# Optimization experiments

Measured on AMD Instinct MI355X. Metric: run time of the kernel, lower is better.

The kernel has to match this reference:

```python
import jax, jax.numpy as jnp
import numpy as np

ITERS = 3

def squash(x, axis=-1):
    norm = jnp.linalg.norm(x, axis=axis, keepdims=True)
    scale = norm ** 2 / (1 + norm ** 2) / (norm + 1e-08)
    return scale * x

def setup_inputs() -> dict:
    key = jax.random.key(0)
    kx, kw = jax.random.split(key)
    x = jax.random.normal(kx, (64, 8000, 8), dtype=jnp.float32)
    W = 0.01 * jax.random.normal(kw, (10, 8000, 16, 8), dtype=jnp.float32)
    return {"x": x, "W": W}

def reference(x, W):
    # u_hat[b,o,i,d] = W[o,i,d,e] @ x[b,i,e]
    u_hat = jnp.einsum('oide,bie->boid', W, x)  # [B, O, I, D]
    temp_u_hat = jax.lax.stop_gradient(u_hat)
    B, O, I, D = u_hat.shape
    b = jnp.zeros((B, O, I, 1), dtype=u_hat.dtype)
    v = jnp.ones((B, O, D), dtype=u_hat.dtype)
    for i in range(ITERS):
        c = jax.nn.softmax(b, axis=1)  # over out_caps
        if i < ITERS - 1:
            s = (c * temp_u_hat).sum(axis=2)       # [B, O, D]
            v = squash(s)
            # agreement: u_hat . v over dim D
            b = b + jnp.einsum('boid,bod->boi', temp_u_hat, v)[..., None]
        else:
            s = (c * u_hat).sum(axis=2)
            v = squash(s)
    return v
```

## Files before the change

### kernel.cpp

```cpp
#include <hip/hip_runtime.h>
#include <hip/hip_fp16.h>
#include <math.h>

#define IN 8000
#define OC 10
#define NUNIT 1000
#define VACC_F (64 * OC * 16)
#define PART_H (64 * OC * 16)

#define REC_B   28672
#define REC_H   14336
#define XOFF_B  20480
#define XOFF_H  10240
#define REC_TOTAL_B ((size_t)NUNIT * REC_B)

#define SM_BYTES 41984

typedef __fp16 h2 __attribute__((ext_vector_type(2)));
typedef _Float16 half8 __attribute__((ext_vector_type(8)));
typedef float f32x16 __attribute__((ext_vector_type(16)));

__device__ __forceinline__ h2 asb(unsigned int v) { return __builtin_bit_cast(h2, v); }

__device__ __forceinline__ float dot2(h2 a, h2 b, float c) {
#if __has_builtin(__builtin_amdgcn_fdot2)
    return __builtin_amdgcn_fdot2(a, b, c, false);
#else
    return fmaf((float)a[0], (float)b[0], fmaf((float)a[1], (float)b[1], c));
#endif
}

__device__ __forceinline__ unsigned int pk_rn(float a, float b) {
    return __builtin_bit_cast(unsigned int, __float22half2_rn(make_float2(a, b)));
}

#define GLDS16(gp, lp) __builtin_amdgcn_global_load_lds(                      \
    (const __attribute__((address_space(1))) void*)(gp),                      \
    (__attribute__((address_space(3))) void*)(lp), 16, 0, 0)

__global__ __launch_bounds__(256) void caps_prep(
    const float* __restrict__ W, const float* __restrict__ x,
    __fp16* __restrict__ rec)
{
    const int t   = threadIdx.x;
    const int blk = blockIdx.x;
    if (blk < 1250) {
        const int gt = blk * 256 + t;
#pragma unroll
        for (int k = 0; k < 4; ++k) {
            int g  = gt + k * 320000;
            int u  = g / 1280;
            int r  = g - u * 1280;
            int il = r / 160;
            int rr = r - il * 160;
            int o  = rr >> 4;
            int d  = rr & 15;
            const float* ip = W + ((size_t)o * IN + (size_t)(u * 8 + il)) * 128 + d * 8;
            float4 f0 = *(const float4*)(ip);
            float4 f1 = *(const float4*)(ip + 4);
            uint4 pk = make_uint4(pk_rn(f0.x, f0.y), pk_rn(f0.z, f0.w),
                                  pk_rn(f1.x, f1.y), pk_rn(f1.z, f1.w));
            *(uint4*)(rec + (size_t)u * REC_H + il * 1280 + o * 128 + d * 8) = pk;
        }
    } else {
        const int u    = (blk - 1250) * 4 + (t >> 6);
        const int lane = t & 63;
#pragma unroll
        for (int il = 0; il < 8; ++il) {
            const float* ip = x + ((size_t)lane * IN + (size_t)(u * 8 + il)) * 8;
            float4 f0 = *(const float4*)(ip);
            float4 f1 = *(const float4*)(ip + 4);
            uint4 pk = make_uint4(pk_rn(f0.x, f0.y), pk_rn(f0.z, f0.w),
                                  pk_rn(f1.x, f1.y), pk_rn(f1.z, f1.w));
            *(uint4*)(rec + (size_t)u * REC_H + XOFF_H + il * 512 + lane * 8) = pk;
        }
    }
}

template<int UNIFORM>
__global__ __launch_bounds__(256, 3) void caps_pass(
    const __fp16* __restrict__ rec, const float* __restrict__ Vacc,
    __fp16* __restrict__ part)
{
    __shared__ __align__(16) unsigned char sm[SM_BYTES];
    __shared__ __align__(16) unsigned char zs[16];

    const int t    = threadIdx.x;
    const int w    = t >> 6;
    const int lane = t & 63;
    const int lo   = lane & 31;
    const int hi   = lane >> 5;
    const int bt   = w & 1;
    const int ph   = w >> 1;
    const int b    = bt * 32 + lo;

    if (t < 4) ((unsigned int*)zs)[t] = 0u;

    h2 vh[10][4];
    if (!UNIFORM) {
        const float* vp = Vacc + (size_t)b * (OC * 16);
        const float L2E = 1.44269504f;
#pragma unroll
        for (int o = 0; o < OC; ++o) {
            float4 fa = *(const float4*)(vp + o * 16 + 4 * hi);
            float4 fb = *(const float4*)(vp + o * 16 + 8 + 4 * hi);
            vh[o][0] = asb(pk_rn(fa.x * L2E, fa.y * L2E));
            vh[o][1] = asb(pk_rn(fa.z * L2E, fa.w * L2E));
            vh[o][2] = asb(pk_rn(fb.x * L2E, fb.y * L2E));
            vh[o][3] = asb(pk_rn(fb.z * L2E, fb.w * L2E));
        }
    }

    f32x16 acc[5];
    h2 acch[5][8];
    if (UNIFORM) {
#pragma unroll
        for (int op = 0; op < 5; ++op)
#pragma unroll
            for (int k = 0; k < 16; ++k) acc[op][k] = 0.f;
    } else {
#pragma unroll
        for (int op = 0; op < 5; ++op)
#pragma unroll
            for (int q = 0; q < 8; ++q) acch[op][q] = h2{(__fp16)0.f, (__fp16)0.f};
    }

    f32x16 zc;
#pragma unroll
    for (int k = 0; k < 16; ++k) zc[k] = 0.f;

    const int bid  = blockIdx.x;
    const int grid = gridDim.x;

    auto issue = [&](int st) {
        const char* g = (const char*)rec + (size_t)st * REC_B + (size_t)lane * 16;
#pragma unroll
        for (int c = 0; c < 7; ++c) {
            const int q = c * 4 + w;
            GLDS16(g + q * 1024, sm + q * 1024);
        }
    };

    bool first = true;
    for (int st = bid; st < NUNIT; st += grid) {
        if (!first) __syncthreads();
        issue(st);
        __syncthreads();
        first = false;

        const unsigned char* buf = sm;

        if (UNIFORM) {
#pragma unroll
            for (int ip = 0; ip < 2; ++ip) {
                const int il0 = ph * 4 + ip * 2;
                half8 xb = *(const half8*)(buf + XOFF_B + (il0 + hi) * 1024 + b * 16);
#pragma unroll
                for (int op = 0; op < 5; ++op) {
                    half8 av = *(const half8*)(buf + (il0 + hi) * 2560 + op * 512 + lo * 16);
                    acc[op] = __builtin_amdgcn_mfma_f32_32x32x16_f16(av, xb, acc[op], 0, 0, 0);
                }
            }
        } else {
#pragma unroll 1
            for (int u = 0; u < 4; ++u) {
                const int il = ph * 4 + u;
                const unsigned char* xaddr = (lane < 32)
                    ? (buf + XOFF_B + il * 1024 + b * 16)
                    : (const unsigned char*)zs;
                half8 xb = *(const half8*)xaddr;

                h2 uh2[5][8];
                float lgf[10];
#pragma unroll
                for (int op = 0; op < 5; ++op) {
                    half8 av = *(const half8*)(buf + il * 2560 + op * 512 + lo * 16);
                    f32x16 C = __builtin_amdgcn_mfma_f32_32x32x16_f16(av, xb, zc, 0, 0, 0);
#pragma unroll
                    for (int q = 0; q < 8; ++q)
                        uh2[op][q] = __builtin_amdgcn_cvt_pkrtz(C[2 * q], C[2 * q + 1]);
                    float l0 = 0.f, l1 = 0.f;
#pragma unroll
                    for (int qq = 0; qq < 4; ++qq) {
                        l0 = dot2(uh2[op][qq],     vh[op * 2][qq],     l0);
                        l1 = dot2(uh2[op][4 + qq], vh[op * 2 + 1][qq], l1);
                    }
                    lgf[op * 2]     = l0;
                    lgf[op * 2 + 1] = l1;
                }
#pragma unroll
                for (int pp = 0; pp < 5; ++pp) {
                    h2 lp = asb(pk_rn(lgf[2 * pp], lgf[2 * pp + 1]));
                    int ob = __shfl_xor(__builtin_bit_cast(int, lp), 32);
                    h2 s2 = lp + __builtin_bit_cast(h2, ob);
                    lgf[2 * pp]     = (float)s2[0];
                    lgf[2 * pp + 1] = (float)s2[1];
                }
                float mx = lgf[0];
#pragma unroll
                for (int o = 1; o < OC; ++o) mx = fmaxf(mx, lgf[o]);
                float pe[10];
                float se = 0.f;
#pragma unroll
                for (int o = 0; o < OC; ++o) {
                    pe[o] = __builtin_amdgcn_exp2f(lgf[o] - mx);
                    se += pe[o];
                }
                float rs = __builtin_amdgcn_rcpf(se);
#pragma unroll
                for (int op = 0; op < 5; ++op) {
                    float c0 = pe[op * 2] * rs;
                    float c1 = pe[op * 2 + 1] * rs;
                    h2 ch0 = __builtin_amdgcn_cvt_pkrtz(c0, c0);
                    h2 ch1 = __builtin_amdgcn_cvt_pkrtz(c1, c1);
#pragma unroll
                    for (int q = 0; q < 4; ++q) {
                        acch[op][q]     = ch0 * uh2[op][q]     + acch[op][q];
                        acch[op][4 + q] = ch1 * uh2[op][4 + q] + acch[op][4 + q];
                    }
                }
            }
        }
    }

    float* red = (float*)sm;
#pragma unroll 1
    for (int phase = 0; phase < 2; ++phase) {
        __syncthreads();
        if (ph == phase) {
#pragma unroll
            for (int op = 0; op < 5; ++op)
#pragma unroll
                for (int q = 0; q < 8; ++q) {
                    const int o  = op * 2 + (q >> 2);
                    const int d0 = 2 * (q & 1) + 8 * ((q >> 1) & 1) + 4 * hi;
                    float e0, e1;
                    if (UNIFORM) { e0 = acc[op][2 * q]; e1 = acc[op][2 * q + 1]; }
                    else         { e0 = (float)acch[op][q][0]; e1 = (float)acch[op][q][1]; }
                    float* p = &red[(size_t)b * 164 + o * 16 + d0];
                    if (phase == 0) {
                        *(float2*)p = make_float2(e0, e1);
                    } else {
                        float2 v2 = *(const float2*)p;
                        v2.x += e0; v2.y += e1;
                        *(float2*)p = v2;
                    }
                }
        }
    }
    __syncthreads();
    unsigned int* dst = (unsigned int*)part;
    for (int q = t; q < PART_H / 2; q += 256) {
        int bo = q >> 3;
        int u8 = q & 7;
        int bb = bo / 10;
        int oo = bo - bb * 10;
        float2 v2 = *(const float2*)&red[(size_t)bb * 164 + oo * 16 + u8 * 2];
        dst[(size_t)(bo * grid + bid) * 8 + u8] = pk_rn(v2.x, v2.y);
    }
}

__global__ __launch_bounds__(256) void caps_reduce(
    const __fp16* __restrict__ part, float* __restrict__ Vacc,
    float* __restrict__ out, int nchunk, int mode, float scale)
{
    const int bo = blockIdx.x;
    const int t  = threadIdx.x;
    const int d2 = t & 3;
    const int s  = t >> 2;

    const unsigned int* p32 = (const unsigned int*)part + (size_t)bo * nchunk * 8;
    float4 a = make_float4(0.f, 0.f, 0.f, 0.f);
    for (int c = s; c < nchunk; c += 64) {
        uint2 v = *(const uint2*)(p32 + (size_t)c * 8 + d2 * 2);
        h2 lov = asb(v.x), hiv = asb(v.y);
        a.x += (float)lov[0]; a.y += (float)lov[1];
        a.z += (float)hiv[0]; a.w += (float)hiv[1];
    }
#pragma unroll
    for (int m = 4; m <= 32; m <<= 1) {
        a.x += __shfl_xor(a.x, m); a.y += __shfl_xor(a.y, m);
        a.z += __shfl_xor(a.z, m); a.w += __shfl_xor(a.w, m);
    }
    __shared__ float red[4][16];
    const int wv = t >> 6;
    if ((t & 63) < 4) {
        red[wv][d2 * 4 + 0] = a.x; red[wv][d2 * 4 + 1] = a.y;
        red[wv][d2 * 4 + 2] = a.z; red[wv][d2 * 4 + 3] = a.w;
    }
    __syncthreads();
    if (t < 16) {
        float sv = (red[0][t] + red[1][t] + red[2][t] + red[3][t]) * scale;
        float n2 = sv * sv;
#pragma unroll
        for (int m = 1; m < 16; m <<= 1) n2 += __shfl_xor(n2, m);
        float norm = sqrtf(n2);
        float scl  = n2 / (1.f + n2) / (norm + 1e-8f);
        float v = scl * sv;
        if (mode == 2)      out[bo * 16 + t] = v;
        else if (mode == 0) Vacc[bo * 16 + t] = v;
        else                Vacc[bo * 16 + t] += v;
    }
}

extern "C" void kernel_launch(void* const* d_in, const int* in_sizes, int n_in,
                              void* d_out, int out_size, void* d_ws, size_t ws_size,
                              hipStream_t stream) {
    const float* x = (const float*)d_in[0];
    const float* W = (const float*)d_in[1];
    float* out = (float*)d_out;

    char* ws = (char*)d_ws;
    float*  Vacc = (float*)ws;
    __fp16* rec  = (__fp16*)(ws + VACC_F * sizeof(float));
    __fp16* part = (__fp16*)(ws + VACC_F * sizeof(float) + REC_TOTAL_B);

    size_t head = VACC_F * sizeof(float) + REC_TOTAL_B;
    size_t avail = (ws_size > head) ? ws_size - head : 0;
    long slots = (long)(avail / (PART_H * sizeof(__fp16)));
    int grid = (int)((slots < NUNIT) ? slots : NUNIT);
    if (grid < 1) grid = 1;

    caps_prep<<<1500, 256, 0, stream>>>(W, x, rec);

    caps_pass<1><<<grid, 256, 0, stream>>>(rec, Vacc, part);
    caps_reduce<<<640, 256, 0, stream>>>(part, Vacc, out, grid, 0, 0.1f);
    caps_pass<0><<<grid, 256, 0, stream>>>(rec, Vacc, part);
    caps_reduce<<<640, 256, 0, stream>>>(part, Vacc, out, grid, 1, 1.0f);
    caps_pass<0><<<grid, 256, 0, stream>>>(rec, Vacc, part);
    caps_reduce<<<640, 256, 0, stream>>>(part, Vacc, out, grid, 2, 1.0f);
}
```

Baseline: 186.8 us.

## Double-buffer LDS record loads in caps_pass and cap the grid at 500 blocks

caps_pass now has two LDS buffers. Each block prefetches its first two units up front and refills a buffer two units ahead after computing on it, instead of doing one load, a barrier and then compute for every unit. The grid is capped at 500 blocks, so each block handles two units and the reduce step has fewer partial slots to sum. Launch bounds drop to 2 blocks per CU to fit the larger LDS footprint. The softmax max and sum reductions are rewritten as shallower trees. The cost is lower occupancy and more LDS per block.

```diff
diff --git a/kernel.cpp b/kernel.cpp
--- a/kernel.cpp
+++ b/kernel.cpp
@@ -13,8 +13,6 @@
 #define XOFF_B  20480
 #define XOFF_H  10240
 #define REC_TOTAL_B ((size_t)NUNIT * REC_B)
-
-#define SM_BYTES 41984
 
 typedef __fp16 h2 __attribute__((ext_vector_type(2)));
 typedef _Float16 half8 __attribute__((ext_vector_type(8)));
@@ -78,11 +76,11 @@
 }
 
 template<int UNIFORM>
-__global__ __launch_bounds__(256, 3) void caps_pass(
+__global__ __launch_bounds__(256, 2) void caps_pass(
     const __fp16* __restrict__ rec, const float* __restrict__ Vacc,
     __fp16* __restrict__ part)
 {
-    __shared__ __align__(16) unsigned char sm[SM_BYTES];
+    __shared__ __align__(16) unsigned char sm[2 * REC_B];
     __shared__ __align__(16) unsigned char zs[16];
 
     const int t    = threadIdx.x;
@@ -132,23 +130,23 @@
     const int bid  = blockIdx.x;
     const int grid = gridDim.x;
 
-    auto issue = [&](int st) {
+    auto issue = [&](int st, int bufi) {
         const char* g = (const char*)rec + (size_t)st * REC_B + (size_t)lane * 16;
+        unsigned char* lb = sm + bufi * REC_B;
 #pragma unroll
         for (int c = 0; c < 7; ++c) {
             const int q = c * 4 + w;
-            GLDS16(g + q * 1024, sm + q * 1024);
+            GLDS16(g + q * 1024, lb + q * 1024);
         }
     };
 
-    bool first = true;
+    issue(bid, 0);
+    if (bid + grid < NUNIT) issue(bid + grid, 1);
+    __syncthreads();
+
+    int cur = 0;
     for (int st = bid; st < NUNIT; st += grid) {
-        if (!first) __syncthreads();
-        issue(st);
-        __syncthreads();
-        first = false;
-
-        const unsigned char* buf = sm;
+        const unsigned char* buf = sm + cur * REC_B;
 
         if (UNIFORM) {
 #pragma unroll
@@ -196,16 +194,18 @@
                     lgf[2 * pp]     = (float)s2[0];
                     lgf[2 * pp + 1] = (float)s2[1];
                 }
-                float mx = lgf[0];
-#pragma unroll
-                for (int o = 1; o < OC; ++o) mx = fmaxf(mx, lgf[o]);
+                float m0 = fmaxf(fmaxf(lgf[0], lgf[1]), lgf[2]);
+                float m1 = fmaxf(fmaxf(lgf[3], lgf[4]), lgf[5]);
+                float m2 = fmaxf(fmaxf(lgf[6], lgf[7]), lgf[8]);
+                float mx = fmaxf(fmaxf(m0, m1), fmaxf(m2, lgf[9]));
                 float pe[10];
-                float se = 0.f;
-#pragma unroll
-                for (int o = 0; o < OC; ++o) {
+#pragma unroll
+                for (int o = 0; o < OC; ++o)
                     pe[o] = __builtin_amdgcn_exp2f(lgf[o] - mx);
-                    se += pe[o];
-                }
+                float s01 = pe[0] + pe[1], s23 = pe[2] + pe[3];
+                float s45 = pe[4] + pe[5], s67 = pe[6] + pe[7];
+                float s89 = pe[8] + pe[9];
+                float se = ((s01 + s23) + (s45 + s67)) + s89;
                 float rs = __builtin_amdgcn_rcpf(se);
 #pragma unroll
                 for (int op = 0; op < 5; ++op) {
@@ -221,6 +221,14 @@
                 }
             }
         }
+
+        const int nxt = st + 2 * grid;
+        if (nxt < NUNIT) {
+            __syncthreads();
+            issue(nxt, cur);
+            __syncthreads();
+        }
+        cur ^= 1;
     }
 
     float* red = (float*)sm;
@@ -318,7 +326,7 @@
     size_t head = VACC_F * sizeof(float) + REC_TOTAL_B;
     size_t avail = (ws_size > head) ? ws_size - head : 0;
     long slots = (long)(avail / (PART_H * sizeof(__fp16)));
-    int grid = (int)((slots < NUNIT) ? slots : NUNIT);
+    int grid = (int)((slots < 500) ? slots : 500);
     if (grid < 1) grid = 1;
 
     caps_prep<<<1500, 256, 0, stream>>>(W, x, rec);
```

Result: faster. 161.6 us (median of 2 runs) (-13.5%).
